# Optimization experiments

Measured on AMD Instinct MI355X. Metric: run time of the kernel, lower is better.

The kernel has to match this reference:

```python
import jax, jax.numpy as jnp
import numpy as np

B, T, D, H = 4, 2048, 512, 8
K = D // H  # head dim = 64

def setup_inputs() -> dict:
    key = jax.random.key(0)
    k1, k2, k3, k4 = jax.random.split(key, 4)
    x = jax.random.normal(k1, (B, T, D), dtype=jnp.float32)
    # torch nn.Linear stores weight as [out_features, in_features]
    w_qkv = jax.random.normal(k2, (3 * D, D), dtype=jnp.float32) * (D ** -0.5)
    w_proj = jax.random.normal(k3, (D, D), dtype=jnp.float32) * (D ** -0.5)
    b_proj = jax.random.normal(k4, (D,), dtype=jnp.float32) * 0.01
    return {"x": x, "w_qkv": w_qkv, "w_proj": w_proj, "b_proj": b_proj}

def reference(x, w_qkv, w_proj, b_proj):
    Bx, Tx, Dx = x.shape
    # qkv projection (no bias): [B,T,3D]
    qkv = jnp.einsum('btd,ed->bte', x, w_qkv)
    q, k, v = jnp.split(qkv, 3, axis=-1)
    # [B,H,T,K]
    def heads(t):
        return t.reshape(Bx, Tx, H, K).transpose(0, 2, 1, 3)
    q, k, v = heads(q), heads(k), heads(v)
    # scaled scores with causal mask
    scores = jnp.einsum('bhqk,bhsk->bhqs', q, k) * (K ** -0.5)  # [B,H,T,T]
    causal = jnp.tril(jnp.ones((Tx, Tx), dtype=bool))
    scores = jnp.where(causal, scores, -jnp.inf)
    attn = jax.nn.softmax(scores, axis=-1)  # dropout p=0.0 -> identity
    out = jnp.einsum('bhqs,bhsk->bhqk', attn, v)  # [B,H,T,K]
    out = out.transpose(0, 2, 1, 3).reshape(Bx, Tx, Dx)
    out = jnp.einsum('btd,ed->bte', out, w_proj) + b_proj
    return out
```

## Files before the change

kernel.cpp:

```cpp
#include <hip/hip_runtime.h>
#include <hip/hip_bf16.h>


typedef unsigned short u16;
typedef __attribute__((ext_vector_type(8))) __bf16 bf16x8;
typedef __attribute__((ext_vector_type(8))) unsigned short u16x8;
typedef __attribute__((ext_vector_type(4))) unsigned short u16x4;
typedef __attribute__((ext_vector_type(4))) float f32x4;
typedef __attribute__((ext_vector_type(4))) unsigned u32x4;
typedef __attribute__((ext_vector_type(2))) unsigned u32x2;

#define DEV static __device__ __forceinline__

DEV void async16(const u16* g, u16* l) {
  __builtin_amdgcn_global_load_lds(
      (const __attribute__((address_space(1))) unsigned int*)g,
      (__attribute__((address_space(3))) unsigned int*)l, 16, 0, 0);
}
DEV u16x8 gld8(const u16* p) { return *(const u16x8*)p; }
DEV void lst8(u16* p, u16x8 v) { *(u16x8*)p = v; }
DEV bf16x8 ldsld8(const u16* p) {
  return __builtin_bit_cast(bf16x8, *(const u16x8*)p);
}
DEV f32x4 mfma16(bf16x8 a, bf16x8 b, f32x4 c) {
  return __builtin_amdgcn_mfma_f32_16x16x32_bf16(a, b, c, 0, 0, 0);
}
DEV u16 f2b(float f) {
  unsigned u = __builtin_bit_cast(unsigned, f);
  u += 0x7FFFu + ((u >> 16) & 1u);
  return (u16)(u >> 16);
}
DEV unsigned pk2(float x, float y) {
  __hip_bfloat162 t = __float22bfloat162_rn(float2{x, y});
  unsigned r;
  __builtin_memcpy(&r, &t, 4);
  return r;
}
DEV u16x8 pack8(f32x4 a, f32x4 b) {
  u32x4 t;
  t[0] = pk2(a[0], a[1]);
  t[1] = pk2(a[2], a[3]);
  t[2] = pk2(b[0], b[1]);
  t[3] = pk2(b[2], b[3]);
  return __builtin_bit_cast(u16x8, t);
}

__global__ void cvt_all(const float* __restrict__ x, const float* __restrict__ wq,
                        u16* __restrict__ xb, u16* __restrict__ wqb) {
  constexpr long NX = 8192L * 512 / 8;
  constexpr long NQ = 1536L * 512 / 8;
  const long i = (long)blockIdx.x * 256 + threadIdx.x;
  if (i < NX) {
    const float* p = x + i * 8;
    *(u16x8*)(xb + i * 8) = pack8(*(const f32x4*)p, *(const f32x4*)(p + 4));
  } else if (i < NX + NQ) {
    const long j = i - NX;
    const float* p = wq + j * 8;
    *(u16x8*)(wqb + j * 8) = pack8(*(const f32x4*)p, *(const f32x4*)(p + 4));
  }
}

__global__ void gemm_bb(const u16* __restrict__ A, const u16* __restrict__ Bt,
                        u16* __restrict__ qb, u16* __restrict__ kT,
                        u16* __restrict__ vT, int K) {
  __shared__ __align__(16) u16 smem[17408];
  auto As = (u16(*)[128 * 32])smem;
  auto Bs = (u16(*)[128 * 32])(smem + 8192);
  u16* Cs = smem;
  constexpr int LDC = 136;

  const int t = threadIdx.x, lane = t & 63, w = t >> 6;
  const int lane15 = lane & 15, quad = lane >> 4;
  const int wr = w >> 1, wc = w & 1;

  const int i = blockIdx.x;
  const int rt = (i & 7) | (((i >> 3) & 7) << 3);
  const int ct = i >> 6;
  const long row0 = (long)rt * 128;
  const int col0 = ct * 128;

  const int srow = w * 16 + (lane >> 2);
  const int scol = (lane & 3) * 8;
  const u16* Ag = A + (row0 + srow) * (long)K + scol;
  const u16* Bg = Bt + ((long)col0 + srow) * (long)K + scol;

  f32x4 acc[4][4];
#pragma unroll
  for (int ii = 0; ii < 4; ii++)
#pragma unroll
    for (int j = 0; j < 4; j++) acc[ii][j] = (f32x4)(0.0f);

  for (int k0 = 0; k0 < K; k0 += 64) {
    __syncthreads();
#pragma unroll
    for (int r = 0; r < 2; r++)
#pragma unroll
      for (int hf = 0; hf < 2; hf++) {
        async16(Ag + (long)r * 64 * K + k0 + hf * 32,
                &As[hf][(r * 64 + w * 16) * 32]);
        async16(Bg + (long)r * 64 * K + k0 + hf * 32,
                &Bs[hf][(r * 64 + w * 16) * 32]);
      }
    __syncthreads();

#pragma unroll
    for (int hf = 0; hf < 2; hf++) {
      bf16x8 a[4], b[4];
#pragma unroll
      for (int ii = 0; ii < 4; ii++)
        a[ii] = ldsld8(&As[hf][(wr * 64 + ii * 16 + lane15) * 32 + quad * 8]);
#pragma unroll
      for (int j = 0; j < 4; j++)
        b[j] = ldsld8(&Bs[hf][(wc * 64 + j * 16 + lane15) * 32 + quad * 8]);
#pragma unroll
      for (int ii = 0; ii < 4; ii++)
#pragma unroll
        for (int j = 0; j < 4; j++) acc[ii][j] = mfma16(a[ii], b[j], acc[ii][j]);
    }
  }

  __syncthreads();

  const long bb = row0 >> 11;
  const int s0g = (int)(row0 & 2047);

  if (col0 >= 1024) {
#pragma unroll
    for (int ii = 0; ii < 4; ii++)
#pragma unroll
      for (int j = 0; j < 4; j++) {
        const int d = wc * 64 + j * 16 + lane15;
        const int sl = wr * 64 + ii * 16 + quad * 4;
        const int psl =
            (sl & ~31) | (((sl >> 2) & 3) << 3) | (((sl >> 4) & 1) << 2);
        u32x2 pr;
        pr[0] = pk2(acc[ii][j][0], acc[ii][j][1]);
        pr[1] = pk2(acc[ii][j][2], acc[ii][j][3]);
        *(u16x4*)&Cs[d * LDC + psl] = __builtin_bit_cast(u16x4, pr);
      }
    __syncthreads();
    const int rr = t >> 4, cc = (t & 15) * 8;
#pragma unroll
    for (int p = 0; p < 8; p++) {
      const int d = p * 16 + rr;
      *(u16x8*)(vT + ((bb * 512 + col0 - 1024 + d) * 2048L) + s0g + cc) =
          *(const u16x8*)&Cs[d * LDC + cc];
    }
  } else {
    const bool isQ = (col0 < 512);
    const float sc = isQ ? 0.18033688f : 1.0f;
#pragma unroll
    for (int ii = 0; ii < 4; ii++)
#pragma unroll
      for (int j = 0; j < 4; j++) {
        const int c = wc * 64 + j * 16 + lane15;
#pragma unroll
        for (int r = 0; r < 4; r++) {
          const int rw = wr * 64 + ii * 16 + quad * 4 + r;
          Cs[rw * LDC + c] = f2b(acc[ii][j][r] * sc);
        }
      }
    __syncthreads();
    const int rr = t >> 4, cc = (t & 15) * 8;
    if (isQ) {
#pragma unroll
      for (int p = 0; p < 8; p++) {
        const int rw = p * 16 + rr;
        *(u16x8*)(qb + (row0 + rw) * 512L + col0 + cc) =
            *(const u16x8*)&Cs[rw * LDC + cc];
      }
    } else {
      const int hbase = (col0 - 512) >> 6;
      const int head = hbase + (cc >> 6);
      const int d0 = cc & 63;
#pragma unroll
      for (int p = 0; p < 8; p++) {
        const int rw = p * 16 + rr;
        *(u16x8*)(kT + ((bb * 8 + head) * 2048L + s0g + rw) * 64 + d0) =
            *(const u16x8*)&Cs[rw * LDC + cc];
      }
    }
  }
}

__global__ void gemm_b64(const u16* __restrict__ A, const float* __restrict__ Bt,
                         const float* __restrict__ bias, float* __restrict__ C,
                         int N, int K) {
  __shared__ __align__(16) u16 smem[17408];
  auto As = (u16(*)[128 * 32])smem;
  auto Bs = (u16(*)[64 * 32])(smem + 8192);
  float* Cs = (float*)smem;
  constexpr int LDCF = 68;

  const int t = threadIdx.x, lane = t & 63, w = t >> 6;
  const int lane15 = lane & 15, quad = lane >> 4;
  const int wr = w >> 1, wc = w & 1;

  const int i = blockIdx.x;
  const int rt = (i & 7) | (((i >> 3) & 7) << 3);
  const int ct = i >> 6;
  const long row0 = (long)rt * 128;
  const int col0 = ct * 64;

  const int srow = w * 16 + (lane >> 2);
  const int scol = (lane & 3) * 8;
  const u16* Ag = A + (row0 + srow) * (long)K + scol;

  const int brow = t >> 2, bc = (t & 3) * 16;
  const float* Bg = Bt + (long)(col0 + brow) * K + bc;
  u16* BsD = &Bs[bc >> 5][brow * 32 + (bc & 31)];

  f32x4 acc[4][2];
#pragma unroll
  for (int ii = 0; ii < 4; ii++)
#pragma unroll
    for (int j = 0; j < 2; j++) acc[ii][j] = (f32x4)(0.0f);

  f32x4 q0 = *(const f32x4*)Bg, q1 = *(const f32x4*)(Bg + 4);
  f32x4 q2 = *(const f32x4*)(Bg + 8), q3 = *(const f32x4*)(Bg + 12);

  for (int k0 = 0; k0 < K; k0 += 64) {
    __syncthreads();
#pragma unroll
    for (int r = 0; r < 2; r++)
#pragma unroll
      for (int hf = 0; hf < 2; hf++)
        async16(Ag + (long)r * 64 * K + k0 + hf * 32,
                &As[hf][(r * 64 + w * 16) * 32]);
    lst8(BsD, pack8(q0, q1));
    lst8(BsD + 8, pack8(q2, q3));
    __syncthreads();

    {
      const int kp = (k0 + 64 < K) ? k0 + 64 : k0;
      q0 = *(const f32x4*)(Bg + kp);     q1 = *(const f32x4*)(Bg + kp + 4);
      q2 = *(const f32x4*)(Bg + kp + 8); q3 = *(const f32x4*)(Bg + kp + 12);
    }

#pragma unroll
    for (int hf = 0; hf < 2; hf++) {
      bf16x8 a[4], b[2];
#pragma unroll
      for (int ii = 0; ii < 4; ii++)
        a[ii] = ldsld8(&As[hf][(wr * 64 + ii * 16 + lane15) * 32 + quad * 8]);
#pragma unroll
      for (int j = 0; j < 2; j++)
        b[j] = ldsld8(&Bs[hf][(wc * 32 + j * 16 + lane15) * 32 + quad * 8]);
#pragma unroll
      for (int ii = 0; ii < 4; ii++)
#pragma unroll
        for (int j = 0; j < 2; j++) acc[ii][j] = mfma16(a[ii], b[j], acc[ii][j]);
    }
  }

  __syncthreads();
#pragma unroll
  for (int ii = 0; ii < 4; ii++)
#pragma unroll
    for (int j = 0; j < 2; j++) {
      const int c = wc * 32 + j * 16 + lane15;
      const float bv = bias[col0 + c];
#pragma unroll
      for (int r = 0; r < 4; r++) {
        const int rw = wr * 64 + ii * 16 + quad * 4 + r;
        Cs[rw * LDCF + c] = acc[ii][j][r] + bv;
      }
    }
  __syncthreads();
  const int rr = t >> 4, cc = (t & 15) * 4;
#pragma unroll
  for (int p = 0; p < 8; p++) {
    const int rw = p * 16 + rr;
    *(f32x4*)(C + (row0 + rw) * (long)N + col0 + cc) =
        *(const f32x4*)&Cs[rw * LDCF + cc];
  }
}

__global__ void __launch_bounds__(512, 4)
attn_v13(const u16* __restrict__ Q, const u16* __restrict__ Kt,
         const u16* __restrict__ Vt, u16* __restrict__ out) {
  constexpr int T = 2048;
  __shared__ __align__(16) u16 Ks[2][2][64 * 72];
  __shared__ __align__(16) u16 Vs[2][2][64 * 72];

  const int t = threadIdx.x, lane = t & 63, w = t >> 6;
  const int lane15 = lane & 15, quad = lane >> 4;
  const int half = w >> 2, wl = w & 3;

  const int i = blockIdx.x;
  int qbi = i & 15;
  if (i >= 256) qbi = 15 - qbi;
  const int h = (i >> 4) & 7;
  const int b = (i >> 7) & 3;
  const u16* kTb = Kt + ((long)b * 8 + h) * 2048 * 64;
  const u16* vTb = Vt + ((long)b * 512 + h * 64) * 2048;

  const u16* gq =
      Q + ((long)b * T + qbi * 128 + wl * 32 + lane15) * 512 + h * 64 + quad * 8;
  const bf16x8 qa0 = __builtin_bit_cast(bf16x8, *(const u16x8*)gq);
  const bf16x8 qa1 = __builtin_bit_cast(bf16x8, *(const u16x8*)(gq + 32));
  const bf16x8 qc0 = __builtin_bit_cast(bf16x8, *(const u16x8*)(gq + 16 * 512));
  const bf16x8 qc1 =
      __builtin_bit_cast(bf16x8, *(const u16x8*)(gq + 16 * 512 + 32));

  const int th = t & 255;
  const int srow = th >> 3, sc8 = (th & 7) * 8;
  const int nsbh = qbi + 1;
  const int s0 = half * nsbh;
  const int sbd = 2 * qbi + (wl >> 1);

  const u16* gk = kTb + (long)(s0 * 64 + srow) * 64 + sc8;
  const u16* gv = vTb + (long)srow * 2048 + s0 * 64 + sc8;

  u16x8 kr0, kr1, vr0, vr1;
  kr0 = gld8(gk); kr1 = gld8(gk + 32 * 64);
  vr0 = gld8(gv); vr1 = gld8(gv + (long)32 * 2048);
  lst8(&Ks[half][0][srow * 72 + sc8], kr0);
  lst8(&Ks[half][0][(srow + 32) * 72 + sc8], kr1);
  lst8(&Vs[half][0][srow * 72 + sc8], vr0);
  lst8(&Vs[half][0][(srow + 32) * 72 + sc8], vr1);
  if (nsbh > 1) { gk += 64 * 64; gv += 64; }
  kr0 = gld8(gk); kr1 = gld8(gk + 32 * 64);
  vr0 = gld8(gv); vr1 = gld8(gv + (long)32 * 2048);

  f32x4 o0[4], o1[4], lsum0 = (f32x4)(0.0f), lsum1 = (f32x4)(0.0f);
#pragma unroll
  for (int j = 0; j < 4; j++) { o0[j] = (f32x4)(0.0f); o1[j] = (f32x4)(0.0f); }

  const bf16x8 ones = __builtin_bit_cast(bf16x8, (u16x8)((u16)0x3F80));
  const int ql0 = ((wl & 1) << 5) + lane15;

  for (int it = 0; it < nsbh; ++it) {
    const u16* Kc = Ks[half][it & 1];
    const u16* Vc = Vs[half][it & 1];
    u16* Kn = Ks[half][(it + 1) & 1];
    u16* Vn = Vs[half][(it + 1) & 1];

    __syncthreads();

    lst8(&Kn[srow * 72 + sc8], kr0);
    lst8(&Kn[(srow + 32) * 72 + sc8], kr1);
    lst8(&Vn[srow * 72 + sc8], vr0);
    lst8(&Vn[(srow + 32) * 72 + sc8], vr1);

    if (it + 2 < nsbh) { gk += 64 * 64; gv += 64; }
    kr0 = gld8(gk); kr1 = gld8(gk + 32 * 64);
    vr0 = gld8(gv); vr1 = gld8(gv + (long)32 * 2048);

    const int sb = s0 + it;
    if (sb <= sbd) {
      __builtin_amdgcn_s_setprio(1);
      f32x4 sf0[4], sf1[4];
#pragma unroll
      for (int j = 0; j < 4; j++) {
        const bf16x8 k0 = ldsld8(&Kc[(j * 16 + lane15) * 72 + quad * 8]);
        const bf16x8 k1 = ldsld8(&Kc[(j * 16 + lane15) * 72 + quad * 8 + 32]);
        sf0[j] = mfma16(k1, qa1, mfma16(k0, qa0, (f32x4)(0.0f)));
        sf1[j] = mfma16(k1, qc1, mfma16(k0, qc0, (f32x4)(0.0f)));
      }

#pragma unroll
      for (int j = 0; j < 4; j++)
#pragma unroll
        for (int r = 0; r < 4; r++) {
          sf0[j][r] = exp2f(sf0[j][r]);
          sf1[j][r] = exp2f(sf1[j][r]);
        }
      if (sb == sbd) {
#pragma unroll
        for (int j = 0; j < 4; j++)
#pragma unroll
          for (int r = 0; r < 4; r++) {
            const int sl = j * 16 + quad * 4 + r;
            if (sl > ql0) sf0[j][r] = 0.0f;
            if (sl > ql0 + 16) sf1[j][r] = 0.0f;
          }
      }

      u32x4 w0, w1, w2, w3;
      w0[0] = pk2(sf0[0][0], sf0[0][1]); w0[1] = pk2(sf0[0][2], sf0[0][3]);
      w0[2] = pk2(sf0[1][0], sf0[1][1]); w0[3] = pk2(sf0[1][2], sf0[1][3]);
      w1[0] = pk2(sf0[2][0], sf0[2][1]); w1[1] = pk2(sf0[2][2], sf0[2][3]);
      w1[2] = pk2(sf0[3][0], sf0[3][1]); w1[3] = pk2(sf0[3][2], sf0[3][3]);
      w2[0] = pk2(sf1[0][0], sf1[0][1]); w2[1] = pk2(sf1[0][2], sf1[0][3]);
      w2[2] = pk2(sf1[1][0], sf1[1][1]); w2[3] = pk2(sf1[1][2], sf1[1][3]);
      w3[0] = pk2(sf1[2][0], sf1[2][1]); w3[1] = pk2(sf1[2][2], sf1[2][3]);
      w3[2] = pk2(sf1[3][0], sf1[3][1]); w3[3] = pk2(sf1[3][2], sf1[3][3]);
      const bf16x8 pa0 = __builtin_bit_cast(bf16x8, w0);
      const bf16x8 pa1 = __builtin_bit_cast(bf16x8, w1);
      const bf16x8 pc0 = __builtin_bit_cast(bf16x8, w2);
      const bf16x8 pc1 = __builtin_bit_cast(bf16x8, w3);

#pragma unroll
      for (int j = 0; j < 4; j++) {
        const int d0 = (j * 16 + lane15) * 72;
        const bf16x8 v0 = ldsld8(&Vc[d0 + quad * 8]);
        const bf16x8 v1 = ldsld8(&Vc[d0 + quad * 8 + 32]);
        o0[j] = mfma16(pa1, v1, mfma16(pa0, v0, o0[j]));
        o1[j] = mfma16(pc1, v1, mfma16(pc0, v0, o1[j]));
      }
      lsum0 = mfma16(pa1, ones, mfma16(pa0, ones, lsum0));
      lsum1 = mfma16(pc1, ones, mfma16(pc0, ones, lsum1));
      __builtin_amdgcn_s_setprio(0);
    }
  }

  __syncthreads();
  float* cmb = (float*)&Ks[0][0][0];
  float* cl = (float*)&Vs[0][0][0];

  if (half == 1) {
    const int q0 = wl * 32 + quad * 4;
#pragma unroll
    for (int j = 0; j < 4; j++)
#pragma unroll
      for (int r = 0; r < 4; r++) {
        cmb[(q0 + r) * 64 + j * 16 + lane15] = o0[j][r];
        cmb[(q0 + 16 + r) * 64 + j * 16 + lane15] = o1[j][r];
      }
    if (lane15 == 0) {
#pragma unroll
      for (int r = 0; r < 4; r++) {
        cl[q0 + r] = lsum0[r];
        cl[q0 + 16 + r] = lsum1[r];
      }
    }
  }
  __syncthreads();

  if (half == 0) {
    const int q0 = wl * 32 + quad * 4;
    f32x4 inv0, inv1;
#pragma unroll
    for (int r = 0; r < 4; r++) {
      inv0[r] = 1.0f / (lsum0[r] + cl[q0 + r]);
      inv1[r] = 1.0f / (lsum1[r] + cl[q0 + 16 + r]);
    }
    const long orow0 = (long)b * T + qbi * 128 + wl * 32;
#pragma unroll
    for (int j = 0; j < 4; j++)
#pragma unroll
      for (int r = 0; r < 4; r++) {
        const float a0 = o0[j][r] + cmb[(q0 + r) * 64 + j * 16 + lane15];
        const float a1 = o1[j][r] + cmb[(q0 + 16 + r) * 64 + j * 16 + lane15];
        const long rr = orow0 + quad * 4 + r;
        out[rr * 512 + h * 64 + j * 16 + lane15] = f2b(a0 * inv0[r]);
        out[(rr + 16) * 512 + h * 64 + j * 16 + lane15] = f2b(a1 * inv1[r]);
      }
  }
}

extern "C" void kernel_launch(void* const* d_in, const int* in_sizes, int n_in,
                              void* d_out, int out_size, void* d_ws, size_t ws_size,
                              hipStream_t stream) {
  const float* x      = (const float*)d_in[0];
  const float* w_qkv  = (const float*)d_in[1];
  const float* w_proj = (const float*)d_in[2];
  const float* b_proj = (const float*)d_in[3];
  float* out = (float*)d_out;

  u16* qb = (u16*)d_ws;
  u16* kT = qb + (size_t)8192 * 512;
  u16* vT = kT + (size_t)32 * 2048 * 64;
  u16* xb = vT + (size_t)32 * 64 * 2048;
  u16* wqb = (u16*)d_out;

  cvt_all<<<2432, 256, 0, stream>>>(x, w_qkv, xb, wqb);
  gemm_bb<<<768, 256, 0, stream>>>(xb, wqb, qb, kT, vT, 512);
  attn_v13<<<512, 512, 0, stream>>>(qb, kT, vT, xb);
  gemm_b64<<<512, 256, 0, stream>>>(xb, w_proj, b_proj, out, 512, 512);
}
```

Baseline: 145.7 us.

## Fuse x fp32-to-bf16 conversion into QKV GEMM A-tile loading

Removes the separate conversion pass over x. The QKV GEMM now reads fp32 x directly, prefetches the next K-slice into registers and packs it to bf16 into LDS, while only the weight conversion remains as a small kernel. The GEMM barriers are replaced by a barrier that waits only on lgkmcnt, and the kT epilogue store mapping is changed so each thread writes 64-element rows per head. This saves a full write and read of x in bf16, at the cost of more registers and synchronous global loads inside the GEMM.

```diff
diff --git a/kernel.cpp b/kernel.cpp
--- a/kernel.cpp
+++ b/kernel.cpp
@@ -44,23 +44,19 @@
   t[3] = pk2(b[2], b[3]);
   return __builtin_bit_cast(u16x8, t);
 }
-
-__global__ void cvt_all(const float* __restrict__ x, const float* __restrict__ wq,
-                        u16* __restrict__ xb, u16* __restrict__ wqb) {
-  constexpr long NX = 8192L * 512 / 8;
-  constexpr long NQ = 1536L * 512 / 8;
-  const long i = (long)blockIdx.x * 256 + threadIdx.x;
-  if (i < NX) {
-    const float* p = x + i * 8;
-    *(u16x8*)(xb + i * 8) = pack8(*(const f32x4*)p, *(const f32x4*)(p + 4));
-  } else if (i < NX + NQ) {
-    const long j = i - NX;
-    const float* p = wq + j * 8;
-    *(u16x8*)(wqb + j * 8) = pack8(*(const f32x4*)p, *(const f32x4*)(p + 4));
-  }
-}
-
-__global__ void gemm_bb(const u16* __restrict__ A, const u16* __restrict__ Bt,
+DEV void barrier_lgkm() {
+  asm volatile("s_waitcnt lgkmcnt(0)" ::: "memory");
+  __builtin_amdgcn_s_barrier();
+  asm volatile("" ::: "memory");
+}
+
+__global__ void cvt_w(const float* __restrict__ wq, u16* __restrict__ wqb) {
+  const long j = (long)blockIdx.x * 256 + threadIdx.x;
+  const float* p = wq + j * 8;
+  *(u16x8*)(wqb + j * 8) = pack8(*(const f32x4*)p, *(const f32x4*)(p + 4));
+}
+
+__global__ void gemm_bb(const float* __restrict__ X, const u16* __restrict__ Bt,
                         u16* __restrict__ qb, u16* __restrict__ kT,
                         u16* __restrict__ vT, int K) {
   __shared__ __align__(16) u16 smem[17408];
@@ -81,8 +77,9 @@
 
   const int srow = w * 16 + (lane >> 2);
   const int scol = (lane & 3) * 8;
-  const u16* Ag = A + (row0 + srow) * (long)K + scol;
+  const float* Xg = X + (row0 + srow) * (long)K + scol;
   const u16* Bg = Bt + ((long)col0 + srow) * (long)K + scol;
+  u16* AsD = &As[0][srow * 32 + scol];
 
   f32x4 acc[4][4];
 #pragma unroll
@@ -90,18 +87,41 @@
 #pragma unroll
     for (int j = 0; j < 4; j++) acc[ii][j] = (f32x4)(0.0f);
 
+  f32x4 ax[8];
+#pragma unroll
+  for (int r = 0; r < 2; r++)
+#pragma unroll
+    for (int hf = 0; hf < 2; hf++) {
+      ax[r * 4 + hf * 2] = *(const f32x4*)(Xg + (long)r * 64 * K + hf * 32);
+      ax[r * 4 + hf * 2 + 1] =
+          *(const f32x4*)(Xg + (long)r * 64 * K + hf * 32 + 4);
+    }
+
   for (int k0 = 0; k0 < K; k0 += 64) {
-    __syncthreads();
+    barrier_lgkm();
 #pragma unroll
     for (int r = 0; r < 2; r++)
 #pragma unroll
       for (int hf = 0; hf < 2; hf++) {
-        async16(Ag + (long)r * 64 * K + k0 + hf * 32,
-                &As[hf][(r * 64 + w * 16) * 32]);
         async16(Bg + (long)r * 64 * K + k0 + hf * 32,
                 &Bs[hf][(r * 64 + w * 16) * 32]);
+        lst8(AsD + hf * 4096 + r * 2048,
+             pack8(ax[r * 4 + hf * 2], ax[r * 4 + hf * 2 + 1]));
       }
     __syncthreads();
+
+    {
+      const int kp = (k0 + 64 < K) ? k0 + 64 : k0;
+#pragma unroll
+      for (int r = 0; r < 2; r++)
+#pragma unroll
+        for (int hf = 0; hf < 2; hf++) {
+          ax[r * 4 + hf * 2] =
+              *(const f32x4*)(Xg + (long)r * 64 * K + kp + hf * 32);
+          ax[r * 4 + hf * 2 + 1] =
+              *(const f32x4*)(Xg + (long)r * 64 * K + kp + hf * 32 + 4);
+        }
+    }
 
 #pragma unroll
     for (int hf = 0; hf < 2; hf++) {
@@ -161,8 +181,8 @@
         }
       }
     __syncthreads();
-    const int rr = t >> 4, cc = (t & 15) * 8;
     if (isQ) {
+      const int rr = t >> 4, cc = (t & 15) * 8;
 #pragma unroll
       for (int p = 0; p < 8; p++) {
         const int rw = p * 16 + rr;
@@ -171,13 +191,14 @@
       }
     } else {
       const int hbase = (col0 - 512) >> 6;
-      const int head = hbase + (cc >> 6);
-      const int d0 = cc & 63;
+      const int rowp = t >> 3;
+      const int cc8 = (t & 7) * 8;
 #pragma unroll
       for (int p = 0; p < 8; p++) {
-        const int rw = p * 16 + rr;
-        *(u16x8*)(kT + ((bb * 8 + head) * 2048L + s0g + rw) * 64 + d0) =
-            *(const u16x8*)&Cs[rw * LDC + cc];
+        const int head = hbase + (p >> 2);
+        const int rw = (p & 3) * 32 + rowp;
+        *(u16x8*)(kT + ((bb * 8 + head) * 2048L + s0g + rw) * 64 + cc8) =
+            *(const u16x8*)&Cs[rw * LDC + (p >> 2) * 64 + cc8];
       }
     }
   }
@@ -220,7 +241,7 @@
   f32x4 q2 = *(const f32x4*)(Bg + 8), q3 = *(const f32x4*)(Bg + 12);
 
   for (int k0 = 0; k0 < K; k0 += 64) {
-    __syncthreads();
+    barrier_lgkm();
 #pragma unroll
     for (int r = 0; r < 2; r++)
 #pragma unroll
@@ -462,11 +483,11 @@
   u16* qb = (u16*)d_ws;
   u16* kT = qb + (size_t)8192 * 512;
   u16* vT = kT + (size_t)32 * 2048 * 64;
-  u16* xb = vT + (size_t)32 * 64 * 2048;
+  u16* ao = vT + (size_t)32 * 64 * 2048;
   u16* wqb = (u16*)d_out;
 
-  cvt_all<<<2432, 256, 0, stream>>>(x, w_qkv, xb, wqb);
-  gemm_bb<<<768, 256, 0, stream>>>(xb, wqb, qb, kT, vT, 512);
-  attn_v13<<<512, 512, 0, stream>>>(qb, kT, vT, xb);
-  gemm_b64<<<512, 256, 0, stream>>>(xb, w_proj, b_proj, out, 512, 512);
-}
+  cvt_w<<<384, 256, 0, stream>>>(w_qkv, wqb);
+  gemm_bb<<<768, 256, 0, stream>>>(x, wqb, qb, kT, vT, 512);
+  attn_v13<<<512, 512, 0, stream>>>(qb, kT, vT, ao);
+  gemm_b64<<<512, 256, 0, stream>>>(ao, w_proj, b_proj, out, 512, 512);
+}
```

Result: no change. 146.0 us (+0.2%).
